# Optimization experiments

Measured on AMD Instinct MI355X. Metric: run time of the kernel, lower is better.

## Reference

```python
import jax, jax.numpy as jnp
import numpy as np

N_NODES = 50000
N_EDGES = 800000
D = 64  # in_dim = hidden = out_dim
LEAKY_SLOPE = 0.01  # F.leaky_relu default


def gat_layer(h, src, dst, W, b, aW, ab):
    # fc: z = h @ W.T + b            [N, D_out]
    z = h @ W.T + b
    zs = z[src]                       # gather src feats  [E, D_out]
    zd = z[dst]                       # gather dst feats  [E, D_out]
    # attn_fc(concat(z_src, z_dst)) -> scalar per edge, then leaky_relu
    e = jnp.concatenate([zs, zd], axis=-1) @ aW.T + ab   # [E, 1]
    e = jax.nn.leaky_relu(e, LEAKY_SLOPE)[:, 0]          # [E]
    # softmax over incoming edges per destination node (mailbox softmax)
    m = jax.ops.segment_max(e, dst, num_segments=N_NODES)    # [N]
    ex = jnp.exp(e - m[dst])
    den = jax.ops.segment_sum(ex, dst, num_segments=N_NODES)  # [N]
    alpha = ex / den[dst]                                      # [E]
    # scatter-sum aggregate of alpha * z_src
    return jax.ops.segment_sum(alpha[:, None] * zs, dst, num_segments=N_NODES)


def setup_inputs() -> dict:
    key = jax.random.key(0)
    ks = jax.random.split(key, 16)
    x = jax.random.normal(ks[0], (N_NODES, D), dtype=jnp.float32)
    src = jax.random.randint(ks[1], (N_EDGES,), 0, N_NODES)
    dst = jax.random.randint(ks[2], (N_EDGES,), 0, N_NODES)
    # xavier_normal with relu gain, per reset_parameters
    gain = float(np.sqrt(2.0))
    params = {}
    for i in range(3):
        std_fc = gain * np.sqrt(2.0 / (D + D))
        std_at = gain * np.sqrt(2.0 / (2 * D + 1))
        params[f"W{i}"] = jax.random.normal(ks[3 + 4 * i], (D, D), dtype=jnp.float32) * std_fc
        params[f"b{i}"] = jnp.zeros((D,), dtype=jnp.float32)
        params[f"a{i}"] = jax.random.normal(ks[4 + 4 * i], (1, 2 * D), dtype=jnp.float32) * std_at
        params[f"ab{i}"] = jnp.zeros((1,), dtype=jnp.float32)
    return {"x": x, "src": src, "dst": dst, **params}


def reference(x, src, dst, W0, b0, a0, ab0, W1, b1, a1, ab1, W2, b2, a2, ab2):
    h = gat_layer(x, src, dst, W0, b0, a0, ab0)
    h = jax.nn.relu(h)
    h = gat_layer(h, src, dst, W1, b1, a1, ab1)
    h = jax.nn.relu(h)
    h = gat_layer(h, src, dst, W2, b2, a2, ab2)
    return h
```

## Files before the change

kernel.cpp:

```cpp
#include <hip/hip_runtime.h>
#include <math.h>

#define N_NODES 50000
#define N_EDGES 800000
#define D 64

#define NB 256
#define NBLK 256
#define BUCKET_NODES 196
#define TILE 3125

typedef unsigned short ushort_t;

__device__ __forceinline__ ushort_t f32_to_bf16(float f) {
    unsigned u = __float_as_uint(f);
    u += 0x7fffu + ((u >> 16) & 1u);
    return (ushort_t)(u >> 16);
}

template<int N>
__global__ void scan_partial_g(const int* __restrict__ in, int* __restrict__ partials) {
    const int base = blockIdx.x * 1024 + threadIdx.x * 4;
    int4 c = make_int4(0, 0, 0, 0);
    if (base + 3 < N) c = *(const int4*)&in[base];
    else { int* cp = (int*)&c; for (int j = 0; j < 4; ++j) if (base + j < N) cp[j] = in[base + j]; }
    int s = c.x + c.y + c.z + c.w;
    #pragma unroll
    for (int off = 32; off >= 1; off >>= 1) s += __shfl_xor(s, off, 64);
    __shared__ int red[4];
    if ((threadIdx.x & 63) == 0) red[threadIdx.x >> 6] = s;
    __syncthreads();
    if (threadIdx.x == 0) partials[blockIdx.x] = red[0] + red[1] + red[2] + red[3];
}

__global__ void scan_offsets_g(int* __restrict__ partials, int nt, int* __restrict__ total_out) {
    const int lane = threadIdx.x;
    const int v = (lane < nt) ? partials[lane] : 0;
    int inc = v;
    #pragma unroll
    for (int off = 1; off < 64; off <<= 1) {
        const int w = __shfl_up(inc, off, 64);
        if (lane >= off) inc += w;
    }
    if (lane < nt) partials[lane] = inc - v;
    if (total_out != nullptr && lane == 63) *total_out = inc;
}

template<int N>
__global__ void scan_write_g(const int* __restrict__ in, const int* __restrict__ partials,
                             int* __restrict__ out) {
    const int tid  = threadIdx.x;
    const int base = blockIdx.x * 1024 + tid * 4;
    int4 c = make_int4(0, 0, 0, 0);
    if (base + 3 < N) c = *(const int4*)&in[base];
    else { int* cp = (int*)&c; for (int j = 0; j < 4; ++j) if (base + j < N) cp[j] = in[base + j]; }
    const int s = c.x + c.y + c.z + c.w;
    __shared__ int sh[256];
    sh[tid] = s;
    __syncthreads();
    for (int off = 1; off < 256; off <<= 1) {
        const int w = (tid >= off) ? sh[tid - off] : 0;
        __syncthreads();
        sh[tid] += w;
        __syncthreads();
    }
    int run = partials[blockIdx.x] + sh[tid] - s;
    const int* cp = (const int*)&c;
    int rp[4];
    #pragma unroll
    for (int j = 0; j < 4; ++j) { rp[j] = run; run += cp[j]; }
    if (base + 3 < N) *(int4*)&out[base] = make_int4(rp[0], rp[1], rp[2], rp[3]);
    else for (int j = 0; j < 4; ++j) if (base + j < N) out[base + j] = rp[j];
}

__global__ __launch_bounds__(256) void bucket_hist(const int* __restrict__ dst,
                                                   int* __restrict__ Acnt) {
    __shared__ int hist[NB];
    for (int i = threadIdx.x; i < NB; i += 256) hist[i] = 0;
    __syncthreads();
    const int base = blockIdx.x * TILE;
    for (int i = threadIdx.x; i < TILE; i += 256)
        atomicAdd(&hist[dst[base + i] / BUCKET_NODES], 1);
    __syncthreads();
    for (int bk = threadIdx.x; bk < NB; bk += 256)
        Acnt[bk * NBLK + blockIdx.x] = hist[bk];
}

__global__ __launch_bounds__(256) void bucket_scatter(const int* __restrict__ src,
                                                      const int* __restrict__ dst,
                                                      const int* __restrict__ offs,
                                                      int2* __restrict__ staging) {
    __shared__ int cur[NB];
    for (int i = threadIdx.x; i < NB; i += 256) cur[i] = offs[i * NBLK + blockIdx.x];
    __syncthreads();
    const int base = blockIdx.x * TILE;
    for (int i = threadIdx.x; i < TILE; i += 256) {
        const int s = src[base + i], d = dst[base + i];
        const int pos = atomicAdd(&cur[d / BUCKET_NODES], 1);
        staging[pos] = make_int2(s, d);
    }
}

__global__ __launch_bounds__(256) void node_counts(const int2* __restrict__ staging,
                                                   const int* __restrict__ offs,
                                                   int* __restrict__ counts) {
    __shared__ int cnt[BUCKET_NODES];
    const int b = blockIdx.x;
    for (int i = threadIdx.x; i < BUCKET_NODES; i += 256) cnt[i] = 0;
    __syncthreads();
    const int s0 = offs[b * NBLK];
    const int s1 = (b == NB - 1) ? N_EDGES : offs[(b + 1) * NBLK];
    for (int i = s0 + threadIdx.x; i < s1; i += 256)
        atomicAdd(&cnt[staging[i].y - b * BUCKET_NODES], 1);
    __syncthreads();
    for (int i = threadIdx.x; i < BUCKET_NODES; i += 256) {
        const int node = b * BUCKET_NODES + i;
        if (node < N_NODES) counts[node] = cnt[i];
    }
}

__global__ __launch_bounds__(256) void bucket_to_csr(const int2* __restrict__ staging,
                                                     const int* __restrict__ offs,
                                                     const int* __restrict__ row_ptr,
                                                     int* __restrict__ csr_src) {
    __shared__ int cur[BUCKET_NODES];
    const int b = blockIdx.x;
    for (int i = threadIdx.x; i < BUCKET_NODES; i += 256) {
        const int node = b * BUCKET_NODES + i;
        cur[i] = (node < N_NODES) ? row_ptr[node] : 0;
    }
    __syncthreads();
    const int s0 = offs[b * NBLK];
    const int s1 = (b == NB - 1) ? N_EDGES : offs[(b + 1) * NBLK];
    for (int i = s0 + threadIdx.x; i < s1; i += 256) {
        const int2 e = staging[i];
        const int pos = atomicAdd(&cur[e.y - b * BUCKET_NODES], 1);
        csr_src[pos] = e.x;
    }
}

__global__ void hist_kernel(const int* __restrict__ dst, int* __restrict__ counts) {
    const int i = blockIdx.x * blockDim.x + threadIdx.x;
    if (i < N_EDGES) atomicAdd(&counts[dst[i]], 1);
}
__global__ void copy_kernel(const int* __restrict__ in, int* __restrict__ out, int n) {
    const int i = blockIdx.x * blockDim.x + threadIdx.x;
    if (i < n) out[i] = in[i];
}
__global__ void scatter_kernel(const int* __restrict__ src, const int* __restrict__ dst,
                               int* __restrict__ cursor, int* __restrict__ csr_src) {
    const int i = blockIdx.x * blockDim.x + threadIdx.x;
    if (i >= N_EDGES) return;
    const int pos = atomicAdd(&cursor[dst[i]], 1);
    csr_src[pos] = src[i];
}

#define NL_ROWS 8
__global__ __launch_bounds__(256) void node_linear_gemm(
    const float* __restrict__ h, ushort_t* __restrict__ zb,
    const float* __restrict__ W, const float* __restrict__ b,
    const float* __restrict__ a, const float* __restrict__ ab,
    float* __restrict__ s_src, float* __restrict__ s_dst)
{
    __shared__ float Wt[64 * 65];
    for (int idx = threadIdx.x; idx < D * D; idx += 256) {
        const int j = idx >> 6, k = idx & 63;
        Wt[k * 65 + j] = W[idx];
    }
    __syncthreads();

    const int lane = threadIdx.x & 63;
    const int wv   = __builtin_amdgcn_readfirstlane(threadIdx.x >> 6);
    const int row0 = (blockIdx.x * 4 + wv) * NL_ROWS;
    if (row0 >= N_NODES) return;

    const float bj  = b[lane];
    const float alo = a[lane];
    const float ahi = a[64 + lane];

    const float* hr[NL_ROWS];
    #pragma unroll
    for (int r = 0; r < NL_ROWS; ++r) hr[r] = h + (size_t)(row0 + r) * D;

    float acc[NL_ROWS];
    #pragma unroll
    for (int r = 0; r < NL_ROWS; ++r) acc[r] = bj;

    #pragma unroll 4
    for (int k = 0; k < D; ++k) {
        const float wkj = Wt[k * 65 + lane];
        #pragma unroll
        for (int r = 0; r < NL_ROWS; ++r)
            acc[r] = fmaf(hr[r][k], wkj, acc[r]);
    }

    #pragma unroll
    for (int r = 0; r < NL_ROWS; ++r) {
        zb[(size_t)(row0 + r) * D + lane] = f32_to_bf16(acc[r]);
        float u = acc[r] * alo;
        float v = acc[r] * ahi;
        #pragma unroll
        for (int off = 32; off >= 1; off >>= 1) {
            u += __shfl_xor(u, off, 64);
            v += __shfl_xor(v, off, 64);
        }
        if (lane == 0) { s_src[row0 + r] = u; s_dst[row0 + r] = v + ab[0]; }
    }
}

template<bool RELU>
__global__ __launch_bounds__(256) void gat_aggregate(
    const int* __restrict__ row_ptr, const int* __restrict__ csr_src,
    const float* __restrict__ s_src, const float* __restrict__ s_dst,
    const ushort_t* __restrict__ zb, float* __restrict__ out)
{
    __shared__ float sh_ex[4][64];
    __shared__ int   sh_si[4][64];
    const int lane = threadIdx.x & 63;
    const int wv   = threadIdx.x >> 6;
    const int node = blockIdx.x * 4 + wv;
    if (node >= N_NODES) return;
    const int beg = row_ptr[node];
    const int end = row_ptr[node + 1];
    if (beg == end) { out[(size_t)node * D + lane] = 0.f; return; }
    const int half = lane >> 5;
    const int fl   = lane & 31;
    const float sd = s_dst[node];

    float m = -INFINITY;
    float den = 0.f;
    float2 acc[8];
    #pragma unroll
    for (int p = 0; p < 8; ++p) acc[p] = make_float2(0.f, 0.f);

    for (int base = beg; base < end; base += 64) {
        const int n = min(64, end - base);
        const int sidx = (lane < n) ? csr_src[base + lane] : 0;
        float e = -INFINITY;
        if (lane < n) {
            e = s_src[sidx] + sd;
            e = e > 0.f ? e : 0.01f * e;
        }
        float mc = e;
        #pragma unroll
        for (int off = 32; off >= 1; off >>= 1) mc = fmaxf(mc, __shfl_xor(mc, off, 64));
        if (mc > m) {
            const float scale = __expf(m - mc);
            den *= scale;
            #pragma unroll
            for (int p = 0; p < 8; ++p) { acc[p].x *= scale; acc[p].y *= scale; }
            m = mc;
        }
        const float ex = __expf(e - m);
        den += ex;
        sh_ex[wv][lane] = ex;
        sh_si[wv][lane] = sidx;
        for (int t = 0; t < n; t += 16) {
            #pragma unroll
            for (int p = 0; p < 8; ++p) {
                const int ei = t + 2 * p + half;
                const float w = sh_ex[wv][ei];
                const int   s = sh_si[wv][ei];
                const unsigned u = *(const unsigned*)&zb[(size_t)s * D + 2 * fl];
                const float f0 = __uint_as_float(u << 16);
                const float f1 = __uint_as_float(u & 0xffff0000u);
                acc[p].x = fmaf(w, f0, acc[p].x);
                acc[p].y = fmaf(w, f1, acc[p].y);
            }
        }
    }
    #pragma unroll
    for (int off = 32; off >= 1; off >>= 1) den += __shfl_xor(den, off, 64);
    float2 tot = make_float2(0.f, 0.f);
    #pragma unroll
    for (int p = 0; p < 8; ++p) { tot.x += acc[p].x; tot.y += acc[p].y; }
    tot.x += __shfl_xor(tot.x, 32, 64);
    tot.y += __shfl_xor(tot.y, 32, 64);
    float2 v = make_float2(tot.x / den, tot.y / den);
    if (RELU) { v.x = fmaxf(v.x, 0.f); v.y = fmaxf(v.y, 0.f); }
    if (half == 0)
        *(float2*)&out[(size_t)node * D + 2 * fl] = v;
}

extern "C" void kernel_launch(void* const* d_in, const int* in_sizes, int n_in,
                              void* d_out, int out_size, void* d_ws, size_t ws_size,
                              hipStream_t stream) {
    const float* x   = (const float*)d_in[0];
    const int*   src = (const int*)d_in[1];
    const int*   dst = (const int*)d_in[2];
    float* out = (float*)d_out;

    char* wp = (char*)d_ws;
    auto alloc = [&](size_t bytes) -> void* {
        void* p = (void*)wp;
        wp += (bytes + 255) & ~(size_t)255;
        return p;
    };
    ushort_t* zb    = (ushort_t*)alloc((size_t)N_NODES * D * sizeof(ushort_t));
    float* s_src   = (float*)alloc((size_t)N_NODES * sizeof(float));
    float* s_dst   = (float*)alloc((size_t)N_NODES * sizeof(float));
    int*   counts  = (int*)alloc((size_t)N_NODES * sizeof(int));
    int*   row_ptr = (int*)alloc((size_t)(N_NODES + 1) * sizeof(int));
    int*   csr_src = (int*)alloc((size_t)N_EDGES * sizeof(int));
    int*   partA   = (int*)alloc(64 * sizeof(int));
    int*   partB   = (int*)alloc(64 * sizeof(int));
    int*   cursor  = (int*)alloc((size_t)N_NODES * sizeof(int));
    int*   Acnt    = (int*)alloc((size_t)NB * NBLK * sizeof(int));
    int*   offs    = (int*)alloc((size_t)NB * NBLK * sizeof(int));
    int2*  staging = (int2*)alloc((size_t)N_EDGES * sizeof(int2));
    size_t bucket_used = (size_t)(wp - (char*)d_ws);

    const bool use_bucket = (ws_size >= bucket_used);

    if (use_bucket) {
        bucket_hist<<<NBLK, 256, 0, stream>>>(dst, Acnt);
        scan_partial_g<NB * NBLK><<<64, 256, 0, stream>>>(Acnt, partB);
        scan_offsets_g<<<1, 64, 0, stream>>>(partB, 64, nullptr);
        scan_write_g<NB * NBLK><<<64, 256, 0, stream>>>(Acnt, partB, offs);
        bucket_scatter<<<NBLK, 256, 0, stream>>>(src, dst, offs, staging);
        node_counts<<<NB, 256, 0, stream>>>(staging, offs, counts);
        scan_partial_g<N_NODES><<<49, 256, 0, stream>>>(counts, partA);
        scan_offsets_g<<<1, 64, 0, stream>>>(partA, 49, &row_ptr[N_NODES]);
        scan_write_g<N_NODES><<<49, 256, 0, stream>>>(counts, partA, row_ptr);
        bucket_to_csr<<<NB, 256, 0, stream>>>(staging, offs, row_ptr, csr_src);
    } else {
        hipMemsetAsync(counts, 0, (size_t)N_NODES * sizeof(int), stream);
        hist_kernel<<<(N_EDGES + 255) / 256, 256, 0, stream>>>(dst, counts);
        scan_partial_g<N_NODES><<<49, 256, 0, stream>>>(counts, partA);
        scan_offsets_g<<<1, 64, 0, stream>>>(partA, 49, &row_ptr[N_NODES]);
        scan_write_g<N_NODES><<<49, 256, 0, stream>>>(counts, partA, row_ptr);
        copy_kernel<<<(N_NODES + 255) / 256, 256, 0, stream>>>(row_ptr, cursor, N_NODES);
        scatter_kernel<<<(N_EDGES + 255) / 256, 256, 0, stream>>>(src, dst, cursor, csr_src);
    }

    const int grid_k1  = (N_NODES + 4 * NL_ROWS - 1) / (4 * NL_ROWS);
    const int grid_agg = (N_NODES + 3) / 4;

    for (int layer = 0; layer < 3; ++layer) {
        const float* W  = (const float*)d_in[3 + 4 * layer];
        const float* b  = (const float*)d_in[4 + 4 * layer];
        const float* a  = (const float*)d_in[5 + 4 * layer];
        const float* ab = (const float*)d_in[6 + 4 * layer];
        const float* hin = (layer == 0) ? x : out;

        node_linear_gemm<<<grid_k1, 256, 0, stream>>>(hin, zb, W, b, a, ab, s_src, s_dst);
        if (layer < 2) {
            gat_aggregate<true ><<<grid_agg, 256, 0, stream>>>(row_ptr, csr_src, s_src, s_dst, zb, out);
        } else {
            gat_aggregate<false><<<grid_agg, 256, 0, stream>>>(row_ptr, csr_src, s_src, s_dst, zb, out);
        }
    }
}
```

Measured before the change: 220.2 us.

## Split GAT aggregation into separate edge-softmax and weighted-gather kernels

The fused online-softmax aggregate kernel is split in two. A new edge_softmax kernel handles four nodes per wavefront, 16 lanes each, and writes normalized per-edge weights packed with source indices into an int2 array. A simpler weighted_gather kernel then reads these and accumulates bf16 features with no max tracking or rescaling. The aim is to remove the rescale and reduction overhead and the wasted lanes on low-degree nodes, at the cost of an extra launch per layer and extra global traffic for the raw and weight buffers.

```diff
diff --git a/kernel.cpp b/kernel.cpp
--- a/kernel.cpp
+++ b/kernel.cpp
@@ -208,78 +208,94 @@
     }
 }
 
-template<bool RELU>
-__global__ __launch_bounds__(256) void gat_aggregate(
+__global__ __launch_bounds__(256) void edge_softmax(
     const int* __restrict__ row_ptr, const int* __restrict__ csr_src,
     const float* __restrict__ s_src, const float* __restrict__ s_dst,
+    float* __restrict__ raw, int2* __restrict__ wgtsi)
+{
+    const int lane = threadIdx.x & 63;
+    const int sl   = lane & 15;
+    const int g    = lane >> 4;
+    const int wid  = blockIdx.x * 4 + (threadIdx.x >> 6);
+    const int node = wid * 4 + g;
+    if (node >= N_NODES) return;
+    const int beg = row_ptr[node];
+    const int end = row_ptr[node + 1];
+    if (beg == end) return;
+    const float sd = s_dst[node];
+
+    float m = -INFINITY, den = 0.f;
+    for (int base = beg; base < end; base += 16) {
+        const int n = min(16, end - base);
+        float e = -INFINITY;
+        if (sl < n) {
+            const int s = csr_src[base + sl];
+            e = s_src[s] + sd;
+            e = e > 0.f ? e : 0.01f * e;
+            raw[base + sl] = e;
+        }
+        float mc = e;
+        #pragma unroll
+        for (int off = 8; off >= 1; off >>= 1) mc = fmaxf(mc, __shfl_xor(mc, off, 64));
+        if (mc > m) { den *= __expf(m - mc); m = mc; }
+        float ex = (sl < n) ? __expf(e - m) : 0.f;
+        #pragma unroll
+        for (int off = 8; off >= 1; off >>= 1) ex += __shfl_xor(ex, off, 64);
+        den += ex;
+    }
+    const float inv = 1.f / den;
+    for (int base = beg; base < end; base += 16) {
+        const int n = min(16, end - base);
+        if (sl < n) {
+            const int i = base + sl;
+            const float w = __expf(raw[i] - m) * inv;
+            wgtsi[i] = make_int2(__float_as_int(w), csr_src[i]);
+        }
+    }
+}
+
+template<bool RELU>
+__global__ __launch_bounds__(256) void weighted_gather(
+    const int* __restrict__ row_ptr, const int2* __restrict__ wgtsi,
     const ushort_t* __restrict__ zb, float* __restrict__ out)
 {
-    __shared__ float sh_ex[4][64];
-    __shared__ int   sh_si[4][64];
+    __shared__ int2 sh[4][64];
     const int lane = threadIdx.x & 63;
     const int wv   = threadIdx.x >> 6;
     const int node = blockIdx.x * 4 + wv;
     if (node >= N_NODES) return;
     const int beg = row_ptr[node];
     const int end = row_ptr[node + 1];
-    if (beg == end) { out[(size_t)node * D + lane] = 0.f; return; }
     const int half = lane >> 5;
     const int fl   = lane & 31;
-    const float sd = s_dst[node];
-
-    float m = -INFINITY;
-    float den = 0.f;
+
     float2 acc[8];
     #pragma unroll
     for (int p = 0; p < 8; ++p) acc[p] = make_float2(0.f, 0.f);
 
     for (int base = beg; base < end; base += 64) {
         const int n = min(64, end - base);
-        const int sidx = (lane < n) ? csr_src[base + lane] : 0;
-        float e = -INFINITY;
-        if (lane < n) {
-            e = s_src[sidx] + sd;
-            e = e > 0.f ? e : 0.01f * e;
-        }
-        float mc = e;
-        #pragma unroll
-        for (int off = 32; off >= 1; off >>= 1) mc = fmaxf(mc, __shfl_xor(mc, off, 64));
-        if (mc > m) {
-            const float scale = __expf(m - mc);
-            den *= scale;
-            #pragma unroll
-            for (int p = 0; p < 8; ++p) { acc[p].x *= scale; acc[p].y *= scale; }
-            m = mc;
-        }
-        const float ex = __expf(e - m);
-        den += ex;
-        sh_ex[wv][lane] = ex;
-        sh_si[wv][lane] = sidx;
+        sh[wv][lane] = (lane < n) ? wgtsi[base + lane] : make_int2(0, 0);
         for (int t = 0; t < n; t += 16) {
             #pragma unroll
             for (int p = 0; p < 8; ++p) {
                 const int ei = t + 2 * p + half;
-                const float w = sh_ex[wv][ei];
-                const int   s = sh_si[wv][ei];
-                const unsigned u = *(const unsigned*)&zb[(size_t)s * D + 2 * fl];
-                const float f0 = __uint_as_float(u << 16);
-                const float f1 = __uint_as_float(u & 0xffff0000u);
-                acc[p].x = fmaf(w, f0, acc[p].x);
-                acc[p].y = fmaf(w, f1, acc[p].y);
+                const int2 ws = sh[wv][ei];
+                const float w = __int_as_float(ws.x);
+                const unsigned u = *(const unsigned*)&zb[(size_t)ws.y * D + 2 * fl];
+                acc[p].x = fmaf(w, __uint_as_float(u << 16), acc[p].x);
+                acc[p].y = fmaf(w, __uint_as_float(u & 0xffff0000u), acc[p].y);
             }
         }
     }
-    #pragma unroll
-    for (int off = 32; off >= 1; off >>= 1) den += __shfl_xor(den, off, 64);
     float2 tot = make_float2(0.f, 0.f);
     #pragma unroll
     for (int p = 0; p < 8; ++p) { tot.x += acc[p].x; tot.y += acc[p].y; }
     tot.x += __shfl_xor(tot.x, 32, 64);
     tot.y += __shfl_xor(tot.y, 32, 64);
-    float2 v = make_float2(tot.x / den, tot.y / den);
-    if (RELU) { v.x = fmaxf(v.x, 0.f); v.y = fmaxf(v.y, 0.f); }
+    if (RELU) { tot.x = fmaxf(tot.x, 0.f); tot.y = fmaxf(tot.y, 0.f); }
     if (half == 0)
-        *(float2*)&out[(size_t)node * D + 2 * fl] = v;
+        *(float2*)&out[(size_t)node * D + 2 * fl] = tot;
 }
 
 extern "C" void kernel_launch(void* const* d_in, const int* in_sizes, int n_in,
@@ -296,7 +312,7 @@
         wp += (bytes + 255) & ~(size_t)255;
         return p;
     };
-    ushort_t* zb    = (ushort_t*)alloc((size_t)N_NODES * D * sizeof(ushort_t));
+    ushort_t* zb   = (ushort_t*)alloc((size_t)N_NODES * D * sizeof(ushort_t));
     float* s_src   = (float*)alloc((size_t)N_NODES * sizeof(float));
     float* s_dst   = (float*)alloc((size_t)N_NODES * sizeof(float));
     int*   counts  = (int*)alloc((size_t)N_NODES * sizeof(int));
@@ -304,6 +320,8 @@
     int*   csr_src = (int*)alloc((size_t)N_EDGES * sizeof(int));
     int*   partA   = (int*)alloc(64 * sizeof(int));
     int*   partB   = (int*)alloc(64 * sizeof(int));
+    float* raw     = (float*)alloc((size_t)N_EDGES * sizeof(float));
+    int2*  wgtsi   = (int2*)alloc((size_t)N_EDGES * sizeof(int2));
     int*   cursor  = (int*)alloc((size_t)N_NODES * sizeof(int));
     int*   Acnt    = (int*)alloc((size_t)NB * NBLK * sizeof(int));
     int*   offs    = (int*)alloc((size_t)NB * NBLK * sizeof(int));
@@ -334,6 +352,7 @@
     }
 
     const int grid_k1  = (N_NODES + 4 * NL_ROWS - 1) / (4 * NL_ROWS);
+    const int grid_sm  = (N_NODES + 15) / 16;
     const int grid_agg = (N_NODES + 3) / 4;
 
     for (int layer = 0; layer < 3; ++layer) {
@@ -344,10 +363,11 @@
         const float* hin = (layer == 0) ? x : out;
 
         node_linear_gemm<<<grid_k1, 256, 0, stream>>>(hin, zb, W, b, a, ab, s_src, s_dst);
+        edge_softmax<<<grid_sm, 256, 0, stream>>>(row_ptr, csr_src, s_src, s_dst, raw, wgtsi);
         if (layer < 2) {
-            gat_aggregate<true ><<<grid_agg, 256, 0, stream>>>(row_ptr, csr_src, s_src, s_dst, zb, out);
+            weighted_gather<true ><<<grid_agg, 256, 0, stream>>>(row_ptr, wgtsi, zb, out);
         } else {
-            gat_aggregate<false><<<grid_agg, 256, 0, stream>>>(row_ptr, csr_src, s_src, s_dst, zb, out);
-        }
-    }
-}
+            weighted_gather<false><<<grid_agg, 256, 0, stream>>>(row_ptr, wgtsi, zb, out);
+        }
+    }
+}
```

Measured after the change: 210.8 us. -4.3%, faster.
